# Performance work log

Measured on AMD Instinct MI355X. Metric: run time of the kernel, lower is better.

The kernel has to match this reference:

```python
import jax, jax.numpy as jnp
import numpy as np

D_MODEL = 1024
N_HEADS = 16
HEAD_DIM = D_MODEL // N_HEADS  # 64, even (required by RoPE)
ROPE_THETA = 10000.0
EPS = 1e-6
PAD_VAL = 1.0


def setup_inputs() -> dict:
    key = jax.random.key(0)
    ks = jax.random.split(key, 5)
    w_scale = 1.0 / np.sqrt(D_MODEL)
    return {
        "x": jax.random.normal(ks[0], (4, 4096, D_MODEL), jnp.float32),
        "Wq": jax.random.normal(ks[1], (D_MODEL, D_MODEL), jnp.float32) * w_scale,
        "Wk": jax.random.normal(ks[2], (D_MODEL, D_MODEL), jnp.float32) * w_scale,
        "Wv": jax.random.normal(ks[3], (D_MODEL, D_MODEL), jnp.float32) * w_scale,
        "Wo": jax.random.normal(ks[4], (D_MODEL, D_MODEL), jnp.float32) * w_scale,
    }


def _rope(x, cos, sin):
    # x: [b, h, s, d]; complex multiply on interleaved (even, odd) pairs,
    # matching torch.view_as_complex on reshape(..., -1, 2).
    x1 = x[..., 0::2]
    x2 = x[..., 1::2]
    r1 = x1 * cos - x2 * sin
    r2 = x1 * sin + x2 * cos
    return jnp.stack([r1, r2], axis=-1).reshape(x.shape)


def reference(x, Wq, Wk, Wv, Wo):
    B, S, D = x.shape
    # qkv projections, split heads -> [b, h, s, hd]
    def split_heads(t):
        return t.reshape(B, S, N_HEADS, HEAD_DIM).transpose(0, 2, 1, 3)
    q = split_heads(x @ Wq)
    k = split_heads(x @ Wk)
    v = split_heads(x @ Wv)

    # precompute_freqs_cis: freqs = 1/theta^(2i/d), angles = t * freqs
    freqs = 1.0 / (ROPE_THETA ** (jnp.arange(0, HEAD_DIM, 2, dtype=jnp.float32) / HEAD_DIM))
    ang = jnp.arange(S, dtype=jnp.float32)[:, None] * freqs[None, :]  # [s, hd/2]
    cos = jnp.cos(ang)[None, None]  # [1,1,s,hd/2]
    sin = jnp.sin(ang)[None, None]
    q = _rope(q, cos, sin)
    k = _rope(k, cos, sin)

    # linear_attn_op: ReLU feature maps + padded-value normalization trick
    q = jax.nn.relu(q)
    k = jax.nn.relu(k)
    v_pad = jnp.pad(v, ((0, 0), (0, 0), (0, 0), (0, 1)), constant_values=PAD_VAL)
    # vk: [b, h, d+1, d] -- tiny state, linear complexity in seq
    vk = jnp.einsum('bhke,bhkd->bhed', v_pad, k)
    num = jnp.einsum('bhed,bhld->bhle', vk, q)  # [b, h, s, d+1]
    attn = num[..., :-1] / (num[..., -1:] + EPS)  # [b, h, s, d]

    out = attn.transpose(0, 2, 1, 3).reshape(B, S, D)
    return out @ Wo
```

## Files before the change

kernel.cpp:

```cpp
#include <hip/hip_runtime.h>
#include <stdint.h>

#define GLOBAL_AS __attribute__((address_space(1)))
#define LDS_AS __attribute__((address_space(3)))

typedef float f32x4 __attribute__((ext_vector_type(4)));
typedef short bf16x8 __attribute__((ext_vector_type(8)));

static __device__ __forceinline__ unsigned short f2b(float f) {
  union { float f; unsigned u; } v; v.f = f;
  return (unsigned short)((v.u + 0x7FFFu + ((v.u >> 16) & 1u)) >> 16);
}

static __device__ __forceinline__ void async16(const void* g, void* l) {
  __builtin_amdgcn_global_load_lds((const GLOBAL_AS unsigned int*)g,
                                   (LDS_AS unsigned int*)l, 16, 0, 0);
}

#define BAR() do { __builtin_amdgcn_s_barrier(); __builtin_amdgcn_sched_barrier(0); } while (0)

__global__ void prep_kernel(const float* __restrict__ x,
                            const float* __restrict__ Wq, const float* __restrict__ Wk,
                            const float* __restrict__ Wv, const float* __restrict__ Wo,
                            unsigned short* __restrict__ xb,
                            unsigned short* __restrict__ WcatT, unsigned short* __restrict__ WoT,
                            float* __restrict__ cosT, float* __restrict__ sinT) {
  __shared__ float tile[32][33];
  const int bid = blockIdx.x;
  const int tid = threadIdx.x;
  if (bid < 16384) {
    const int i = bid * 256 + tid;
    float4 v = ((const float4*)x)[i];
    ushort4 o;
    o.x = f2b(v.x); o.y = f2b(v.y); o.z = f2b(v.z); o.w = f2b(v.w);
    ((ushort4*)xb)[i] = o;
  } else if (bid < 16384 + 512) {
    const int idx = (bid - 16384) * 256 + tid;
    const int s = idx >> 5, j = idx & 31;
    float freq = expf(-((float)(2 * j) * (1.0f / 64.0f)) * 9.210340371976184f);
    float ang = (float)s * freq;
    float sn, cs;
    sincosf(ang, &sn, &cs);
    cosT[idx] = cs;
    sinT[idx] = sn;
  } else {
    const int t = bid - 16896;
    const int mat = t >> 10;
    const int r = t & 1023;
    const int k0 = (r & 31) * 32, n0 = (r >> 5) * 32;
    const float* W = (mat == 0) ? Wq : (mat == 1) ? Wk : (mat == 2) ? Wv : Wo;
    unsigned short* WT = (mat < 3) ? (WcatT + (size_t)mat * 1024 * 1024) : WoT;
    const int tx = tid & 31, ty = tid >> 5;
    #pragma unroll
    for (int i = 0; i < 4; i++)
      tile[ty + i * 8][tx] = W[(size_t)(k0 + ty + i * 8) * 1024 + n0 + tx];
    __syncthreads();
    #pragma unroll
    for (int i = 0; i < 4; i++)
      WT[(size_t)(n0 + ty + i * 8) * 1024 + k0 + tx] = f2b(tile[tx][ty + i * 8]);
  }
}

__device__ __forceinline__ void gemm256_core(const unsigned short* __restrict__ Ag,
                                             const unsigned short* __restrict__ Bg,
                                             int m0, int n0, char* lds, f32x4 (&acc)[8][4]) {
  const int tid = threadIdx.x;
  const int lane = tid & 63;
  const int lrow = lane & 15;
  const int quad = lane >> 4;
  const int wave = tid >> 6;
  const int wm = wave >> 2;
  const int wn = wave & 3;

  const unsigned short* Ar0 = Ag + (size_t)m0 * 1024;
  const unsigned short* Ar1 = Ag + (size_t)(m0 + 128) * 1024;
  const unsigned short* Br0 = Bg + (size_t)n0 * 1024;
  const unsigned short* Br1 = Bg + (size_t)(n0 + 128) * 1024;

  auto stage = [&](const unsigned short* src, char* dst) {
    #pragma unroll
    for (int l = 0; l < 2; ++l) {
      const int slot = l * 512 + tid;
      const int row = slot >> 3;
      const int ch = (slot & 7) ^ (row & 7);
      async16(src + (size_t)row * 1024 + ch * 8, dst + slot * 16);
    }
  };

  stage(Ar0, lds);
  stage(Ar1, lds + 16384);
  stage(Br0, lds + 32768);
  stage(Br1, lds + 49152);
  stage(Br0 + 64, lds + 65536 + 32768);
  stage(Br1 + 64, lds + 65536 + 49152);
  asm volatile("s_waitcnt vmcnt(4)" ::: "memory");
  BAR();

  #pragma unroll 1
  for (int t = 0; t < 16; ++t) {
    const int kt = t * 64;
    char* cur = lds + ((t & 1) << 16);
    char* nxt = lds + (((t + 1) & 1) << 16);
    const char* aB = cur + wm * 16384;
    const char* bB = cur + 32768 + (wn >> 1) * 16384;
    const int br0 = (wn & 1) * 64;

    bf16x8 a[4][2], b01[2][2], b23[2][2];

    #pragma unroll
    for (int mt = 0; mt < 4; ++mt) {
      const int r = mt * 16 + lrow;
      #pragma unroll
      for (int kk = 0; kk < 2; ++kk) {
        const int kc = kk * 4 + quad;
        a[mt][kk] = *(const bf16x8*)(aB + r * 128 + ((kc ^ (r & 7)) << 4));
      }
    }
    #pragma unroll
    for (int nt = 0; nt < 2; ++nt) {
      const int r = br0 + nt * 16 + lrow;
      #pragma unroll
      for (int kk = 0; kk < 2; ++kk) {
        const int kc = kk * 4 + quad;
        b01[nt][kk] = *(const bf16x8*)(bB + r * 128 + ((kc ^ (r & 7)) << 4));
      }
    }
    if (t < 15) stage(Ar0 + kt + 64, nxt);
    BAR();
    __builtin_amdgcn_s_setprio(1);
    #pragma unroll
    for (int mt = 0; mt < 4; ++mt)
      #pragma unroll
      for (int nt = 0; nt < 2; ++nt)
        #pragma unroll
        for (int kk = 0; kk < 2; ++kk)
          acc[mt][nt] = __builtin_amdgcn_mfma_f32_16x16x32_bf16(a[mt][kk], b01[nt][kk], acc[mt][nt], 0, 0, 0);
    __builtin_amdgcn_s_setprio(0);
    BAR();

    #pragma unroll
    for (int nt = 0; nt < 2; ++nt) {
      const int r = br0 + (nt + 2) * 16 + lrow;
      #pragma unroll
      for (int kk = 0; kk < 2; ++kk) {
        const int kc = kk * 4 + quad;
        b23[nt][kk] = *(const bf16x8*)(bB + r * 128 + ((kc ^ (r & 7)) << 4));
      }
    }
    if (t < 15) stage(Ar1 + kt + 64, nxt + 16384);
    BAR();
    __builtin_amdgcn_s_setprio(1);
    #pragma unroll
    for (int mt = 0; mt < 4; ++mt)
      #pragma unroll
      for (int nt = 0; nt < 2; ++nt)
        #pragma unroll
        for (int kk = 0; kk < 2; ++kk)
          acc[mt][nt + 2] = __builtin_amdgcn_mfma_f32_16x16x32_bf16(a[mt][kk], b23[nt][kk], acc[mt][nt + 2], 0, 0, 0);
    __builtin_amdgcn_s_setprio(0);
    BAR();

    #pragma unroll
    for (int mt = 0; mt < 4; ++mt) {
      const int r = 64 + mt * 16 + lrow;
      #pragma unroll
      for (int kk = 0; kk < 2; ++kk) {
        const int kc = kk * 4 + quad;
        a[mt][kk] = *(const bf16x8*)(aB + r * 128 + ((kc ^ (r & 7)) << 4));
      }
    }
    if (t < 14) stage(Br0 + kt + 128, cur + 32768);
    BAR();
    __builtin_amdgcn_s_setprio(1);
    #pragma unroll
    for (int mt = 0; mt < 4; ++mt)
      #pragma unroll
      for (int nt = 0; nt < 2; ++nt)
        #pragma unroll
        for (int kk = 0; kk < 2; ++kk)
          acc[mt + 4][nt + 2] = __builtin_amdgcn_mfma_f32_16x16x32_bf16(a[mt][kk], b23[nt][kk], acc[mt + 4][nt + 2], 0, 0, 0);
    __builtin_amdgcn_s_setprio(0);
    BAR();

    if (t < 14) stage(Br1 + kt + 128, cur + 49152);
    BAR();
    __builtin_amdgcn_s_setprio(1);
    #pragma unroll
    for (int mt = 0; mt < 4; ++mt)
      #pragma unroll
      for (int nt = 0; nt < 2; ++nt)
        #pragma unroll
        for (int kk = 0; kk < 2; ++kk)
          acc[mt + 4][nt] = __builtin_amdgcn_mfma_f32_16x16x32_bf16(a[mt][kk], b01[nt][kk], acc[mt + 4][nt], 0, 0, 0);
    __builtin_amdgcn_s_setprio(0);
    if (t < 14)      { asm volatile("s_waitcnt vmcnt(4)" ::: "memory"); }
    else if (t == 14){ asm volatile("s_waitcnt vmcnt(0)" ::: "memory"); }
    BAR();
  }
}

__global__ __launch_bounds__(512, 2)
void gemm_qkv_kernel(const unsigned short* __restrict__ xb,
                     const unsigned short* __restrict__ WT,
                     const float* __restrict__ cosT,
                     const float* __restrict__ sinT,
                     unsigned short* __restrict__ Qd,
                     unsigned short* __restrict__ KTd,
                     unsigned short* __restrict__ VTd) {
  __shared__ char lds[131072];
  const int m0 = blockIdx.x * 256;
  const int n0 = blockIdx.y * 256;

  f32x4 acc[8][4];
  #pragma unroll
  for (int i = 0; i < 8; ++i)
    #pragma unroll
    for (int j = 0; j < 4; ++j) acc[i][j] = (f32x4){0.f, 0.f, 0.f, 0.f};

  gemm256_core(xb, WT, m0, n0, lds, acc);

  const int tid = threadIdx.x;
  const int lane = tid & 63;
  const int lrow = lane & 15;
  const int quad = lane >> 4;
  const int wave = tid >> 6;
  const int wm = wave >> 2;
  const int wn = wave & 3;

  const int b = m0 >> 12;
  const int sec = n0 >> 10;
  const int s0 = (m0 & 4095) + wm * 128;
  const int c0 = (n0 & 1023) + wn * 64;

  if (sec == 2) {
    #pragma unroll
    for (int i = 0; i < 8; ++i) {
      const int sB4 = s0 + i * 16 + quad * 4;
      #pragma unroll
      for (int nt = 0; nt < 4; ++nt) {
        const int c = c0 + nt * 16 + lrow;
        const int h = c >> 6, e = c & 63;
        ushort4 pk;
        pk.x = f2b(acc[i][nt][0]); pk.y = f2b(acc[i][nt][1]);
        pk.z = f2b(acc[i][nt][2]); pk.w = f2b(acc[i][nt][3]);
        *(ushort4*)&VTd[((size_t)(b * 16 + h) * 64 + e) * 4096 + sB4] = pk;
      }
    }
  } else {
    #pragma unroll
    for (int i = 0; i < 8; ++i) {
      const int sB4 = s0 + i * 16 + quad * 4;
      #pragma unroll
      for (int nt = 0; nt < 4; ++nt) {
        const int c = c0 + nt * 16 + lrow;
        const int j = (c & 63) >> 1;
        float ov[4];
        #pragma unroll
        for (int r = 0; r < 4; ++r) {
          const float v = acc[i][nt][r];
          const float p = __shfl_xor(v, 1, 64);
          const int s = sB4 + r;
          const float cs = cosT[s * 32 + j];
          const float sn = sinT[s * 32 + j];
          const float tt = (lane & 1) ? p * sn : -p * sn;
          ov[r] = fmaxf(fmaf(v, cs, tt), 0.0f);
        }
        if (sec == 0) {
          const int grow = m0 + wm * 128 + i * 16 + quad * 4;
          #pragma unroll
          for (int r = 0; r < 4; ++r)
            Qd[(size_t)(grow + r) * 1024 + c] = f2b(ov[r]);
        } else {
          const int h = c >> 6, d = c & 63;
          ushort4 pk;
          pk.x = f2b(ov[0]); pk.y = f2b(ov[1]); pk.z = f2b(ov[2]); pk.w = f2b(ov[3]);
          *(ushort4*)&KTd[((size_t)(b * 16 + h) * 64 + d) * 4096 + sB4] = pk;
        }
      }
    }
  }
}

__global__ __launch_bounds__(256)
void vk_partial_kernel(const unsigned short* __restrict__ KTd,
                       const unsigned short* __restrict__ VTd,
                       float* __restrict__ vkp) {
  __shared__ char sV[4096];
  __shared__ char sK[4096];
  const int tid = threadIdx.x;
  const int lane = tid & 63;
  const int wave = tid >> 6;
  const int lrow = lane & 15;
  const int quad = lane >> 4;
  const int bh = blockIdx.x;
  const int kb = blockIdx.y;
  const int s00 = kb * 512;

  const f32x4 zf = {0.f, 0.f, 0.f, 0.f};
  f32x4 acc[5];
  #pragma unroll
  for (int i = 0; i < 5; i++) acc[i] = zf;

  bf16x8 af4;
  const short oneb = (short)0x3F80;
  #pragma unroll
  for (int j = 0; j < 8; j++) af4[j] = (lrow == 0) ? oneb : (short)0;

  const int srow = tid >> 2;
  const int gcol = ((tid & 3) ^ (srow & 3)) * 8;

  for (int kt = 0; kt < 512; kt += 32) {
    __syncthreads();
    async16(VTd + ((size_t)bh * 64 + srow) * 4096 + s00 + kt + gcol, &sV[tid * 16]);
    async16(KTd + ((size_t)bh * 64 + srow) * 4096 + s00 + kt + gcol, &sK[tid * 16]);
    __syncthreads();
    const int rowK = wave * 16 + lrow;
    bf16x8 bfrag = *(const bf16x8*)&sK[rowK * 64 + ((quad ^ (rowK & 3)) << 4)];
    #pragma unroll
    for (int mt = 0; mt < 4; mt++) {
      const int rowV = mt * 16 + lrow;
      bf16x8 af = *(const bf16x8*)&sV[rowV * 64 + ((quad ^ (rowV & 3)) << 4)];
      acc[mt] = __builtin_amdgcn_mfma_f32_16x16x32_bf16(af, bfrag, acc[mt], 0, 0, 0);
    }
    acc[4] = __builtin_amdgcn_mfma_f32_16x16x32_bf16(af4, bfrag, acc[4], 0, 0, 0);
  }

  #pragma unroll
  for (int mt = 0; mt < 5; mt++) {
    #pragma unroll
    for (int r = 0; r < 4; r++) {
      const int e = mt * 16 + quad * 4 + r;
      const int d = wave * 16 + lrow;
      vkp[((size_t)(bh * 8 + kb) * 80 + e) * 64 + d] = acc[mt][r];
    }
  }
}

__global__ void vk_reduce_kernel(const float* __restrict__ vkp, unsigned short* __restrict__ vkb) {
  int idx = blockIdx.x * 256 + threadIdx.x;
  if (idx >= 64 * 80 * 64) return;
  int bh = idx / 5120, r = idx % 5120;
  float s = 0.f;
  #pragma unroll
  for (int kb = 0; kb < 8; kb++) s += vkp[(size_t)(bh * 8 + kb) * 5120 + r];
  vkb[idx] = f2b(s);
}

__global__ __launch_bounds__(256)
void attn_kernel(const unsigned short* __restrict__ Qd,
                 const unsigned short* __restrict__ vkb,
                 unsigned short* __restrict__ attn) {
  __shared__ char sQ[32768];
  __shared__ char sVK[10240];
  const int tid = threadIdx.x;
  const int lane = tid & 63;
  const int wave = tid >> 6;
  const int lrow = lane & 15;
  const int quad = lane >> 4;
  const int bh = blockIdx.y, b = bh >> 4, h = bh & 15;
  const int l0 = b * 4096 + blockIdx.x * 256;

  const int c4 = tid & 7;
  #pragma unroll
  for (int r = 0; r < 8; r++) {
    const int o = r * 4096 + tid * 16;
    const int row = o >> 7;
    const int g4 = c4 ^ (row & 7);
    async16(Qd + (size_t)(l0 + row) * 1024 + h * 64 + g4 * 8, &sQ[o]);
  }
  {
    int row = tid >> 3;
    int g4 = c4 ^ (row & 7);
    async16(vkb + (size_t)bh * 5120 + row * 64 + g4 * 8, &sVK[tid * 16]);
    row += 32; g4 = c4 ^ (row & 7);
    async16(vkb + (size_t)bh * 5120 + row * 64 + g4 * 8, &sVK[4096 + tid * 16]);
    if (tid < 128) {
      row = 64 + (tid >> 3); g4 = c4 ^ (row & 7);
      async16(vkb + (size_t)bh * 5120 + row * 64 + g4 * 8, &sVK[8192 + tid * 16]);
    }
  }
  __syncthreads();

  const f32x4 zf = {0.f, 0.f, 0.f, 0.f};
  f32x4 acc[4][5];
  #pragma unroll
  for (int i = 0; i < 4; i++)
    #pragma unroll
    for (int j = 0; j < 5; j++) acc[i][j] = zf;

  #pragma unroll
  for (int kk = 0; kk < 2; kk++) {
    const int kc = kk * 4 + quad;
    bf16x8 af[4], bfr[5];
    #pragma unroll
    for (int mt = 0; mt < 4; mt++) {
      const int row = wave * 64 + mt * 16 + lrow;
      af[mt] = *(const bf16x8*)&sQ[row * 128 + ((kc ^ (row & 7)) << 4)];
    }
    #pragma unroll
    for (int nt = 0; nt < 5; nt++) {
      const int row = nt * 16 + lrow;
      bfr[nt] = *(const bf16x8*)&sVK[row * 128 + ((kc ^ (row & 7)) << 4)];
    }
    #pragma unroll
    for (int mt = 0; mt < 4; mt++)
      #pragma unroll
      for (int nt = 0; nt < 5; nt++)
        acc[mt][nt] = __builtin_amdgcn_mfma_f32_16x16x32_bf16(af[mt], bfr[nt], acc[mt][nt], 0, 0, 0);
  }

  #pragma unroll
  for (int mt = 0; mt < 4; mt++) {
    #pragma unroll
    for (int r = 0; r < 4; r++) {
      const float den = __shfl(acc[mt][4][r], lane & 48, 64);
      const float inv = 1.0f / (den + 1e-6f);
      const int l = l0 + wave * 64 + mt * 16 + quad * 4 + r;
      #pragma unroll
      for (int nt = 0; nt < 4; nt++)
        attn[(size_t)l * 1024 + h * 64 + nt * 16 + lrow] = f2b(acc[mt][nt][r] * inv);
    }
  }
}

__global__ __launch_bounds__(512, 2)
void gemm_out_kernel(const unsigned short* __restrict__ A,
                     const unsigned short* __restrict__ BT,
                     float* __restrict__ C) {
  __shared__ char lds[131072];
  const int m0 = blockIdx.x * 256;
  const int n0 = blockIdx.y * 256;

  f32x4 acc[8][4];
  #pragma unroll
  for (int i = 0; i < 8; ++i)
    #pragma unroll
    for (int j = 0; j < 4; ++j) acc[i][j] = (f32x4){0.f, 0.f, 0.f, 0.f};

  gemm256_core(A, BT, m0, n0, lds, acc);

  const int tid = threadIdx.x;
  const int lane = tid & 63;
  const int lrow = lane & 15;
  const int quad = lane >> 4;
  const int wave = tid >> 6;
  const int wm = wave >> 2;
  const int wn = wave & 3;

  const int grow = m0 + wm * 128;
  #pragma unroll
  for (int i = 0; i < 8; ++i) {
    #pragma unroll
    for (int nt = 0; nt < 4; ++nt) {
      const int c = n0 + wn * 64 + nt * 16 + lrow;
      #pragma unroll
      for (int r = 0; r < 4; ++r)
        C[(size_t)(grow + i * 16 + quad * 4 + r) * 1024 + c] = acc[i][nt][r];
    }
  }
}

extern "C" void kernel_launch(void* const* d_in, const int* in_sizes, int n_in,
                              void* d_out, int out_size, void* d_ws, size_t ws_size,
                              hipStream_t stream) {
  const float* x  = (const float*)d_in[0];
  const float* Wq = (const float*)d_in[1];
  const float* Wk = (const float*)d_in[2];
  const float* Wv = (const float*)d_in[3];
  const float* Wo = (const float*)d_in[4];
  float* out = (float*)d_out;

  char* ws = (char*)d_ws;
  size_t off = 0;
  auto alloc = [&](size_t bytes) -> char* {
    char* p = ws + off;
    off += (bytes + 255) & ~(size_t)255;
    return p;
  };

  unsigned short* xb    = (unsigned short*)alloc((size_t)16384 * 1024 * 2);
  unsigned short* WcatT = (unsigned short*)alloc((size_t)3072 * 1024 * 2);
  unsigned short* WoT   = (unsigned short*)alloc((size_t)1024 * 1024 * 2);
  float* cosT           = (float*)alloc((size_t)4096 * 32 * 4);
  float* sinT           = (float*)alloc((size_t)4096 * 32 * 4);
  unsigned short* Qd    = (unsigned short*)alloc((size_t)16384 * 1024 * 2);
  unsigned short* KTd   = (unsigned short*)alloc((size_t)64 * 64 * 4096 * 2);
  unsigned short* VTd   = (unsigned short*)alloc((size_t)64 * 64 * 4096 * 2);
  float* vkp            = (float*)alloc((size_t)512 * 5120 * 4);
  unsigned short* vkb   = (unsigned short*)alloc((size_t)64 * 5120 * 2);
  unsigned short* attn  = xb;

  prep_kernel<<<16384 + 512 + 4096, 256, 0, stream>>>(x, Wq, Wk, Wv, Wo, xb, WcatT, WoT, cosT, sinT);
  gemm_qkv_kernel<<<dim3(64, 12), 512, 0, stream>>>(xb, WcatT, cosT, sinT, Qd, KTd, VTd);
  vk_partial_kernel<<<dim3(64, 8), 256, 0, stream>>>(KTd, VTd, vkp);
  vk_reduce_kernel<<<1280, 256, 0, stream>>>(vkp, vkb);
  attn_kernel<<<dim3(16, 64), 256, 0, stream>>>(Qd, vkb, attn);
  gemm_out_kernel<<<dim3(64, 4), 512, 0, stream>>>(attn, WoT, out);
}
```

Measured before the change: 324.0 us.

## Prefetch next k-tile fragments into registers to overlap LDS reads with MFMA

Restructures the GEMM main loop into a software-pipelined schedule. Before the loop the first A and B register fragments are loaded. Each iteration then reads the next tile's B fragments and first-half A fragments from the other LDS buffer while the current MFMAs run. The global-to-LDS stage calls and vmcnt waits are reordered to fit the new schedule. This aims to hide LDS read latency behind matrix math, at the cost of extra VGPRs for the double-buffered fragments (risking spills or lower occupancy at 512 threads x 2 blocks), plus more delicate wait-count correctness.

```diff
diff --git a/kernel.cpp b/kernel.cpp
--- a/kernel.cpp
+++ b/kernel.cpp
@@ -87,6 +87,8 @@
     }
   };
 
+  const int br0 = (wn & 1) * 64;
+
   stage(Ar0, lds);
   stage(Ar1, lds + 16384);
   stage(Br0, lds + 32768);
@@ -96,106 +98,132 @@
   asm volatile("s_waitcnt vmcnt(4)" ::: "memory");
   BAR();
 
+  bf16x8 aq0[4][2], aq1[4][2], b01[2][2], b23[2][2], b01n[2][2], b23n[2][2];
+
+  {
+    const char* aB = lds + wm * 16384;
+    const char* bB = lds + 32768 + (wn >> 1) * 16384;
+    #pragma unroll
+    for (int mt = 0; mt < 4; ++mt)
+      #pragma unroll
+      for (int kk = 0; kk < 2; ++kk) {
+        const int r = mt * 16 + lrow;
+        const int kc = kk * 4 + quad;
+        aq0[mt][kk] = *(const bf16x8*)(aB + r * 128 + ((kc ^ (r & 7)) << 4));
+      }
+    #pragma unroll
+    for (int nt = 0; nt < 2; ++nt)
+      #pragma unroll
+      for (int kk = 0; kk < 2; ++kk) {
+        const int kc = kk * 4 + quad;
+        const int r1 = br0 + nt * 16 + lrow;
+        b01[nt][kk] = *(const bf16x8*)(bB + r1 * 128 + ((kc ^ (r1 & 7)) << 4));
+        const int r2 = br0 + (nt + 2) * 16 + lrow;
+        b23[nt][kk] = *(const bf16x8*)(bB + r2 * 128 + ((kc ^ (r2 & 7)) << 4));
+      }
+  }
+
   #pragma unroll 1
   for (int t = 0; t < 16; ++t) {
     const int kt = t * 64;
     char* cur = lds + ((t & 1) << 16);
     char* nxt = lds + (((t + 1) & 1) << 16);
-    const char* aB = cur + wm * 16384;
-    const char* bB = cur + 32768 + (wn >> 1) * 16384;
-    const int br0 = (wn & 1) * 64;
-
-    bf16x8 a[4][2], b01[2][2], b23[2][2];
-
-    #pragma unroll
-    for (int mt = 0; mt < 4; ++mt) {
-      const int r = mt * 16 + lrow;
+    const char* aB  = cur + wm * 16384;
+    const char* aBn = nxt + wm * 16384;
+    const char* bBn = nxt + 32768 + (wn >> 1) * 16384;
+
+    if (t < 15) stage(Ar0 + kt + 64, nxt);
+    #pragma unroll
+    for (int mt = 0; mt < 4; ++mt)
       #pragma unroll
       for (int kk = 0; kk < 2; ++kk) {
+        const int r = 64 + mt * 16 + lrow;
         const int kc = kk * 4 + quad;
-        a[mt][kk] = *(const bf16x8*)(aB + r * 128 + ((kc ^ (r & 7)) << 4));
+        aq1[mt][kk] = *(const bf16x8*)(aB + r * 128 + ((kc ^ (r & 7)) << 4));
       }
-    }
-    #pragma unroll
-    for (int nt = 0; nt < 2; ++nt) {
-      const int r = br0 + nt * 16 + lrow;
+    BAR();
+    __builtin_amdgcn_s_setprio(1);
+    #pragma unroll
+    for (int kk = 0; kk < 2; ++kk)
+      #pragma unroll
+      for (int mt = 0; mt < 4; ++mt)
+        #pragma unroll
+        for (int nt = 0; nt < 2; ++nt)
+          acc[mt][nt] = __builtin_amdgcn_mfma_f32_16x16x32_bf16(aq0[mt][kk], b01[nt][kk], acc[mt][nt], 0, 0, 0);
+    __builtin_amdgcn_s_setprio(0);
+    BAR();
+
+    if (t < 15) stage(Ar1 + kt + 64, nxt + 16384);
+    if (t < 15) { asm volatile("s_waitcnt vmcnt(4)" ::: "memory"); }
+    BAR();
+    __builtin_amdgcn_s_setprio(1);
+    #pragma unroll
+    for (int kk = 0; kk < 2; ++kk)
+      #pragma unroll
+      for (int mt = 0; mt < 4; ++mt)
+        #pragma unroll
+        for (int nt = 0; nt < 2; ++nt)
+          acc[mt][nt + 2] = __builtin_amdgcn_mfma_f32_16x16x32_bf16(aq0[mt][kk], b23[nt][kk], acc[mt][nt + 2], 0, 0, 0);
+    __builtin_amdgcn_s_setprio(0);
+    BAR();
+
+    if (t < 14) stage(Br0 + kt + 128, cur + 32768);
+    if (t < 14)      { asm volatile("s_waitcnt vmcnt(2)" ::: "memory"); }
+    else if (t == 14){ asm volatile("s_waitcnt vmcnt(0)" ::: "memory"); }
+    if (t < 15) {
+      #pragma unroll
+      for (int nt = 0; nt < 2; ++nt)
+        #pragma unroll
+        for (int kk = 0; kk < 2; ++kk) {
+          const int kc = kk * 4 + quad;
+          const int r1 = br0 + nt * 16 + lrow;
+          b01n[nt][kk] = *(const bf16x8*)(bBn + r1 * 128 + ((kc ^ (r1 & 7)) << 4));
+          const int r2 = br0 + (nt + 2) * 16 + lrow;
+          b23n[nt][kk] = *(const bf16x8*)(bBn + r2 * 128 + ((kc ^ (r2 & 7)) << 4));
+        }
+    }
+    BAR();
+    __builtin_amdgcn_s_setprio(1);
+    #pragma unroll
+    for (int kk = 0; kk < 2; ++kk)
+      #pragma unroll
+      for (int mt = 0; mt < 4; ++mt)
+        #pragma unroll
+        for (int nt = 0; nt < 2; ++nt)
+          acc[mt + 4][nt + 2] = __builtin_amdgcn_mfma_f32_16x16x32_bf16(aq1[mt][kk], b23[nt][kk], acc[mt + 4][nt + 2], 0, 0, 0);
+    __builtin_amdgcn_s_setprio(0);
+    BAR();
+
+    if (t < 14) stage(Br1 + kt + 128, cur + 49152);
+    if (t < 15) {
+      #pragma unroll
+      for (int mt = 0; mt < 4; ++mt)
+        #pragma unroll
+        for (int kk = 0; kk < 2; ++kk) {
+          const int r = mt * 16 + lrow;
+          const int kc = kk * 4 + quad;
+          aq0[mt][kk] = *(const bf16x8*)(aBn + r * 128 + ((kc ^ (r & 7)) << 4));
+        }
+    }
+    BAR();
+    __builtin_amdgcn_s_setprio(1);
+    #pragma unroll
+    for (int kk = 0; kk < 2; ++kk)
+      #pragma unroll
+      for (int mt = 0; mt < 4; ++mt)
+        #pragma unroll
+        for (int nt = 0; nt < 2; ++nt)
+          acc[mt + 4][nt] = __builtin_amdgcn_mfma_f32_16x16x32_bf16(aq1[mt][kk], b01[nt][kk], acc[mt + 4][nt], 0, 0, 0);
+    __builtin_amdgcn_s_setprio(0);
+    BAR();
+
+    #pragma unroll
+    for (int nt = 0; nt < 2; ++nt)
       #pragma unroll
       for (int kk = 0; kk < 2; ++kk) {
-        const int kc = kk * 4 + quad;
-        b01[nt][kk] = *(const bf16x8*)(bB + r * 128 + ((kc ^ (r & 7)) << 4));
+        b01[nt][kk] = b01n[nt][kk];
+        b23[nt][kk] = b23n[nt][kk];
       }
-    }
-    if (t < 15) stage(Ar0 + kt + 64, nxt);
-    BAR();
-    __builtin_amdgcn_s_setprio(1);
-    #pragma unroll
-    for (int mt = 0; mt < 4; ++mt)
-      #pragma unroll
-      for (int nt = 0; nt < 2; ++nt)
-        #pragma unroll
-        for (int kk = 0; kk < 2; ++kk)
-          acc[mt][nt] = __builtin_amdgcn_mfma_f32_16x16x32_bf16(a[mt][kk], b01[nt][kk], acc[mt][nt], 0, 0, 0);
-    __builtin_amdgcn_s_setprio(0);
-    BAR();
-
-    #pragma unroll
-    for (int nt = 0; nt < 2; ++nt) {
-      const int r = br0 + (nt + 2) * 16 + lrow;
-      #pragma unroll
-      for (int kk = 0; kk < 2; ++kk) {
-        const int kc = kk * 4 + quad;
-        b23[nt][kk] = *(const bf16x8*)(bB + r * 128 + ((kc ^ (r & 7)) << 4));
-      }
-    }
-    if (t < 15) stage(Ar1 + kt + 64, nxt + 16384);
-    BAR();
-    __builtin_amdgcn_s_setprio(1);
-    #pragma unroll
-    for (int mt = 0; mt < 4; ++mt)
-      #pragma unroll
-      for (int nt = 0; nt < 2; ++nt)
-        #pragma unroll
-        for (int kk = 0; kk < 2; ++kk)
-          acc[mt][nt + 2] = __builtin_amdgcn_mfma_f32_16x16x32_bf16(a[mt][kk], b23[nt][kk], acc[mt][nt + 2], 0, 0, 0);
-    __builtin_amdgcn_s_setprio(0);
-    BAR();
-
-    #pragma unroll
-    for (int mt = 0; mt < 4; ++mt) {
-      const int r = 64 + mt * 16 + lrow;
-      #pragma unroll
-      for (int kk = 0; kk < 2; ++kk) {
-        const int kc = kk * 4 + quad;
-        a[mt][kk] = *(const bf16x8*)(aB + r * 128 + ((kc ^ (r & 7)) << 4));
-      }
-    }
-    if (t < 14) stage(Br0 + kt + 128, cur + 32768);
-    BAR();
-    __builtin_amdgcn_s_setprio(1);
-    #pragma unroll
-    for (int mt = 0; mt < 4; ++mt)
-      #pragma unroll
-      for (int nt = 0; nt < 2; ++nt)
-        #pragma unroll
-        for (int kk = 0; kk < 2; ++kk)
-          acc[mt + 4][nt + 2] = __builtin_amdgcn_mfma_f32_16x16x32_bf16(a[mt][kk], b23[nt][kk], acc[mt + 4][nt + 2], 0, 0, 0);
-    __builtin_amdgcn_s_setprio(0);
-    BAR();
-
-    if (t < 14) stage(Br1 + kt + 128, cur + 49152);
-    BAR();
-    __builtin_amdgcn_s_setprio(1);
-    #pragma unroll
-    for (int mt = 0; mt < 4; ++mt)
-      #pragma unroll
-      for (int nt = 0; nt < 2; ++nt)
-        #pragma unroll
-        for (int kk = 0; kk < 2; ++kk)
-          acc[mt + 4][nt] = __builtin_amdgcn_mfma_f32_16x16x32_bf16(a[mt][kk], b01[nt][kk], acc[mt + 4][nt], 0, 0, 0);
-    __builtin_amdgcn_s_setprio(0);
-    if (t < 14)      { asm volatile("s_waitcnt vmcnt(4)" ::: "memory"); }
-    else if (t == 14){ asm volatile("s_waitcnt vmcnt(0)" ::: "memory"); }
-    BAR();
   }
 }
 
```

Result: slower. 587.3 us (+81.3%).
